# Performance work log

Measured on AMD Instinct MI355X. Metric: run time of the kernel, lower is better.

The kernel has to match this reference:

```python
import jax, jax.numpy as jnp
import numpy as np

D_MODEL = 1024
NUM_HEADS = 16
D_HEAD = D_MODEL // NUM_HEADS


def setup_inputs() -> dict:
    key = jax.random.key(0)
    ks = jax.random.split(key, 9)
    s = 1.0 / np.sqrt(D_MODEL)
    x = jax.random.normal(ks[0], (2, 2048, D_MODEL), dtype=jnp.float32)
    # Linear layers: weight [out, in] (torch convention), bias [out]
    w_q = jax.random.uniform(ks[1], (D_MODEL, D_MODEL), jnp.float32, -s, s)
    b_q = jax.random.uniform(ks[2], (D_MODEL,), jnp.float32, -s, s)
    w_k = jax.random.uniform(ks[3], (D_MODEL, D_MODEL), jnp.float32, -s, s)
    b_k = jax.random.uniform(ks[4], (D_MODEL,), jnp.float32, -s, s)
    w_v = jax.random.uniform(ks[5], (D_MODEL, D_MODEL), jnp.float32, -s, s)
    b_v = jax.random.uniform(ks[6], (D_MODEL,), jnp.float32, -s, s)
    w_o = jax.random.uniform(ks[7], (D_MODEL, D_MODEL), jnp.float32, -s, s)
    b_o = jax.random.uniform(ks[8], (D_MODEL,), jnp.float32, -s, s)
    return {"x": x, "w_q": w_q, "b_q": b_q, "w_k": w_k, "b_k": b_k,
            "w_v": w_v, "b_v": b_v, "w_o": w_o, "b_o": b_o}


def _split_heads(t, b, s):
    # [b, s, d_model] -> [b, h, s, d_head]
    return t.reshape(b, s, NUM_HEADS, D_HEAD).transpose(0, 2, 1, 3)


def reference(x, w_q, b_q, w_k, b_k, w_v, b_v, w_o, b_o):
    b, s, _ = x.shape
    q = _split_heads(x @ w_q.T + b_q, b, s)
    k = _split_heads(x @ w_k.T + b_k, b, s)
    v = _split_heads(x @ w_v.T + b_v, b, s)
    scores = jnp.einsum('bhid,bhjd->bhij', q, k) / jnp.sqrt(jnp.float32(D_HEAD)).astype(x.dtype)
    attn = jax.nn.softmax(scores, axis=-1)
    out = jnp.einsum('bhij,bhjd->bhid', attn, v)
    out = out.transpose(0, 2, 1, 3).reshape(b, s, D_MODEL)
    return out @ w_o.T + b_o
```

## Files before the change

### kernel.cpp

```cpp
#include <hip/hip_runtime.h>
#include <cstddef>
#include <cstdint>
#include <cmath>

#define NH   16
#define DH   64
#define SLEN 2048
#define DM   1024

typedef __bf16          bf16x8   __attribute__((ext_vector_type(8)));
typedef float           f32x4    __attribute__((ext_vector_type(4)));
typedef unsigned short  ushort8  __attribute__((ext_vector_type(8)));
typedef unsigned short  ushort4v __attribute__((ext_vector_type(4)));

__device__ __forceinline__ unsigned short f2bf(float x) {
    union { float f; unsigned u; } v; v.f = x;
    unsigned r = v.u + 0x7fffu + ((v.u >> 16) & 1u);
    return (unsigned short)(r >> 16);
}
__device__ __forceinline__ float bf2f(unsigned short h) {
    union { unsigned u; float f; } v; v.u = ((unsigned)h) << 16;
    return v.f;
}

__device__ __forceinline__ f32x4 mfma16(ushort8 a, ushort8 b, f32x4 c) {
    return __builtin_amdgcn_mfma_f32_16x16x32_bf16(
        __builtin_bit_cast(bf16x8, a), __builtin_bit_cast(bf16x8, b), c, 0, 0, 0);
}

__global__ __launch_bounds__(256)
void convert_hilo(const float* __restrict__ x,
                  const float* __restrict__ wq, const float* __restrict__ wk,
                  const float* __restrict__ wv, const float* __restrict__ wo,
                  unsigned short* __restrict__ xh, unsigned short* __restrict__ xl,
                  unsigned short* __restrict__ wh, unsigned short* __restrict__ wl)
{
    const unsigned c = blockIdx.x * 256 + threadIdx.x;
    const float* src;
    unsigned short *dh, *dl;
    size_t off;
    if (c < 1048576u) {
        src = x; dh = xh; dl = xl; off = c;
    } else {
        unsigned t = c - 1048576u;
        unsigned wsel = t >> 18;
        off = t & 262143u;
        src  = (wsel == 0) ? wq : (wsel == 1) ? wk : (wsel == 2) ? wv : wo;
        dh = wh + ((size_t)wsel << 20);
        dl = wl + ((size_t)wsel << 20);
    }
    float4 v = *(const float4*)(src + off * 4);
    float a[4] = {v.x, v.y, v.z, v.w};
    ushort4v h, l;
    #pragma unroll
    for (int i = 0; i < 4; ++i) {
        unsigned short hi = f2bf(a[i]);
        h[i] = hi;
        l[i] = f2bf(a[i] - bf2f(hi));
    }
    *(ushort4v*)(dh + off * 4) = h;
    *(ushort4v*)(dl + off * 4) = l;
}

template<int MODE>
__global__ __launch_bounds__(256, 1)
void gemm_split(const unsigned short* __restrict__ Ahi, const unsigned short* __restrict__ Alo,
                const unsigned short* __restrict__ Whi, const unsigned short* __restrict__ Wlo,
                const float* __restrict__ bias, float* __restrict__ outF,
                unsigned short* __restrict__ outH, unsigned short* __restrict__ outL)
{
    constexpr int K = DM;
    __shared__ unsigned short sAh[128][40], sAl[128][40], sBh[128][40], sBl[128][40];

    const int tid  = threadIdx.x;
    const int bm   = blockIdx.x * 128;
    const int bn   = blockIdx.y * 128;
    const int wid  = tid >> 6;
    const int lane = tid & 63;
    const int wm   = (wid >> 1) * 64;
    const int wn   = (wid & 1) * 64;

    const int r0 = tid >> 2;
    const int c0 = (tid & 3) * 8;

    const unsigned short* pAh0 = Ahi + (size_t)(bm + r0) * K + c0;
    const unsigned short* pAl0 = Alo + (size_t)(bm + r0) * K + c0;
    const unsigned short* pBh0 = Whi + (size_t)(bn + r0) * K + c0;
    const unsigned short* pBl0 = Wlo + (size_t)(bn + r0) * K + c0;
    const size_t rstep = (size_t)64 * K;

    ushort8 vah0 = *(const ushort8*)(pAh0), vah1 = *(const ushort8*)(pAh0 + rstep);
    ushort8 val0 = *(const ushort8*)(pAl0), val1 = *(const ushort8*)(pAl0 + rstep);
    ushort8 vbh0 = *(const ushort8*)(pBh0), vbh1 = *(const ushort8*)(pBh0 + rstep);
    ushort8 vbl0 = *(const ushort8*)(pBl0), vbl1 = *(const ushort8*)(pBl0 + rstep);

    f32x4 acc[4][4];
    #pragma unroll
    for (int i = 0; i < 4; ++i)
        #pragma unroll
        for (int j = 0; j < 4; ++j)
            acc[i][j] = (f32x4)0.0f;

    const int fr = lane & 15;
    const int kq = (lane >> 4) * 8;

    for (int k0 = 0; k0 < K; k0 += 32) {
        __syncthreads();
        *(ushort8*)&sAh[r0][c0]      = vah0;  *(ushort8*)&sAh[r0 + 64][c0] = vah1;
        *(ushort8*)&sAl[r0][c0]      = val0;  *(ushort8*)&sAl[r0 + 64][c0] = val1;
        *(ushort8*)&sBh[r0][c0]      = vbh0;  *(ushort8*)&sBh[r0 + 64][c0] = vbh1;
        *(ushort8*)&sBl[r0][c0]      = vbl0;  *(ushort8*)&sBl[r0 + 64][c0] = vbl1;
        __syncthreads();

        if (k0 + 32 < K) {
            const int kn = k0 + 32;
            vah0 = *(const ushort8*)(pAh0 + kn);  vah1 = *(const ushort8*)(pAh0 + rstep + kn);
            val0 = *(const ushort8*)(pAl0 + kn);  val1 = *(const ushort8*)(pAl0 + rstep + kn);
            vbh0 = *(const ushort8*)(pBh0 + kn);  vbh1 = *(const ushort8*)(pBh0 + rstep + kn);
            vbl0 = *(const ushort8*)(pBl0 + kn);  vbl1 = *(const ushort8*)(pBl0 + rstep + kn);
        }

        ushort8 afh[4], afl[4], bfh[4], bfl[4];
        #pragma unroll
        for (int i = 0; i < 4; ++i) {
            afh[i] = *(const ushort8*)&sAh[wm + i * 16 + fr][kq];
            afl[i] = *(const ushort8*)&sAl[wm + i * 16 + fr][kq];
            bfh[i] = *(const ushort8*)&sBh[wn + i * 16 + fr][kq];
            bfl[i] = *(const ushort8*)&sBl[wn + i * 16 + fr][kq];
        }

        #pragma unroll
        for (int i = 0; i < 4; ++i)
            #pragma unroll
            for (int j = 0; j < 4; ++j) {
                acc[i][j] = mfma16(afh[i], bfh[j], acc[i][j]);
                acc[i][j] = mfma16(afh[i], bfl[j], acc[i][j]);
                acc[i][j] = mfma16(afl[i], bfh[j], acc[i][j]);
            }
    }

    #pragma unroll
    for (int j = 0; j < 4; ++j) {
        const int n = bn + wn + j * 16 + fr;
        const float bs = bias[n];
        #pragma unroll
        for (int i = 0; i < 4; ++i) {
            #pragma unroll
            for (int q = 0; q < 4; ++q) {
                const int m = bm + wm + i * 16 + (lane >> 4) * 4 + q;
                const float v = acc[i][j][q] + bs;
                if (MODE == 0) {
                    outF[(size_t)m * DM + n] = v;
                } else {
                    const int bb = m >> 11, s = m & 2047, hh = n >> 6, dd = n & 63;
                    size_t idx;
                    if (MODE == 1) idx = ((((size_t)bb * NH + hh) * SLEN) + s) * DH + dd;
                    else           idx = ((((size_t)bb * NH + hh) * DH) + dd) * SLEN + s;
                    const unsigned short vh = f2bf(v);
                    outH[idx] = vh;
                    outL[idx] = f2bf(v - bf2f(vh));
                }
            }
        }
    }
}

__global__ __launch_bounds__(256)
void flash_attn_mfma(const unsigned short* __restrict__ Qh, const unsigned short* __restrict__ Ql,
                     const unsigned short* __restrict__ Kh, const unsigned short* __restrict__ Kl,
                     const unsigned short* __restrict__ Vth, const unsigned short* __restrict__ Vtl,
                     unsigned short* __restrict__ Ohi, unsigned short* __restrict__ Olo)
{
    __shared__ unsigned short sKh[64][72], sKl[64][72], sVh[64][72], sVl[64][72];
    __shared__ float sP[4][16][68];

    const int tid  = threadIdx.x;
    const int wid  = tid >> 6;
    const int lane = tid & 63;
    const int fr   = lane & 15;
    const int g    = lane >> 4;
    const int kq   = g * 8;
    const int q0   = blockIdx.x * 64;
    const int h    = blockIdx.y;
    const int b    = blockIdx.z;
    const size_t hb = (((size_t)b) * NH + h) * (size_t)SLEN * DH;

    const int r0 = tid >> 2;
    const int cq = (tid & 3) * 16;

    ushort8 qh[2], ql[2];
    {
        const size_t qbase = hb + (size_t)(q0 + wid * 16 + fr) * DH;
        qh[0] = *(const ushort8*)&Qh[qbase + kq];
        qh[1] = *(const ushort8*)&Qh[qbase + 32 + kq];
        ql[0] = *(const ushort8*)&Ql[qbase + kq];
        ql[1] = *(const ushort8*)&Ql[qbase + 32 + kq];
    }

    float mx[4], li[4];
    f32x4 acc[4];
    #pragma unroll
    for (int r = 0; r < 4; ++r) { mx[r] = -INFINITY; li[r] = 0.0f; }
    #pragma unroll
    for (int j = 0; j < 4; ++j) acc[j] = (f32x4)0.0f;

    for (int t = 0; t < SLEN / 64; ++t) {
        __syncthreads();
        {
            const size_t kbase = hb + (size_t)(t * 64 + r0) * DH + cq;
            *(ushort8*)&sKh[r0][cq]     = *(const ushort8*)&Kh[kbase];
            *(ushort8*)&sKh[r0][cq + 8] = *(const ushort8*)&Kh[kbase + 8];
            *(ushort8*)&sKl[r0][cq]     = *(const ushort8*)&Kl[kbase];
            *(ushort8*)&sKl[r0][cq + 8] = *(const ushort8*)&Kl[kbase + 8];
            const size_t vbase = hb + (size_t)r0 * SLEN + t * 64 + cq;
            *(ushort8*)&sVh[r0][cq]     = *(const ushort8*)&Vth[vbase];
            *(ushort8*)&sVh[r0][cq + 8] = *(const ushort8*)&Vth[vbase + 8];
            *(ushort8*)&sVl[r0][cq]     = *(const ushort8*)&Vtl[vbase];
            *(ushort8*)&sVl[r0][cq + 8] = *(const ushort8*)&Vtl[vbase + 8];
        }
        __syncthreads();

        f32x4 s[4];
        #pragma unroll
        for (int j = 0; j < 4; ++j) s[j] = (f32x4)0.0f;
        #pragma unroll
        for (int j = 0; j < 4; ++j) {
            #pragma unroll
            for (int ks = 0; ks < 2; ++ks) {
                ushort8 kfh = *(const ushort8*)&sKh[j * 16 + fr][ks * 32 + kq];
                ushort8 kfl = *(const ushort8*)&sKl[j * 16 + fr][ks * 32 + kq];
                s[j] = mfma16(qh[ks], kfh, s[j]);
                s[j] = mfma16(qh[ks], kfl, s[j]);
                s[j] = mfma16(ql[ks], kfh, s[j]);
            }
        }

        float p[4][4];
        #pragma unroll
        for (int r = 0; r < 4; ++r) {
            float sc[4];
            float rm = -INFINITY;
            #pragma unroll
            for (int j = 0; j < 4; ++j) { sc[j] = s[j][r] * 0.125f; rm = fmaxf(rm, sc[j]); }
            #pragma unroll
            for (int off = 1; off < 16; off <<= 1)
                rm = fmaxf(rm, __shfl_xor(rm, off));
            const float mn   = fmaxf(mx[r], rm);
            const float corr = __expf(mx[r] - mn);
            mx[r] = mn;
            float rs = 0.0f;
            #pragma unroll
            for (int j = 0; j < 4; ++j) { p[r][j] = __expf(sc[j] - mn); rs += p[r][j]; }
            #pragma unroll
            for (int off = 1; off < 16; off <<= 1)
                rs += __shfl_xor(rs, off);
            li[r] = li[r] * corr + rs;
            #pragma unroll
            for (int j = 0; j < 4; ++j) acc[j][r] *= corr;
        }

        #pragma unroll
        for (int r = 0; r < 4; ++r)
            #pragma unroll
            for (int j = 0; j < 4; ++j)
                sP[wid][g * 4 + r][j * 16 + fr] = p[r][j];

        #pragma unroll
        for (int ks = 0; ks < 2; ++ks) {
            float4 pa = *(const float4*)&sP[wid][fr][ks * 32 + kq];
            float4 pb = *(const float4*)&sP[wid][fr][ks * 32 + kq + 4];
            float pe[8] = {pa.x, pa.y, pa.z, pa.w, pb.x, pb.y, pb.z, pb.w};
            ushort8 ph, pl;
            #pragma unroll
            for (int e = 0; e < 8; ++e) {
                const unsigned short hh = f2bf(pe[e]);
                ph[e] = hh;
                pl[e] = f2bf(pe[e] - bf2f(hh));
            }
            #pragma unroll
            for (int j = 0; j < 4; ++j) {
                ushort8 vfh = *(const ushort8*)&sVh[j * 16 + fr][ks * 32 + kq];
                ushort8 vfl = *(const ushort8*)&sVl[j * 16 + fr][ks * 32 + kq];
                acc[j] = mfma16(ph, vfh, acc[j]);
                acc[j] = mfma16(ph, vfl, acc[j]);
                acc[j] = mfma16(pl, vfh, acc[j]);
            }
        }
    }

    #pragma unroll
    for (int r = 0; r < 4; ++r) {
        const float inv = 1.0f / li[r];
        const int q = q0 + wid * 16 + g * 4 + r;
        const size_t base = ((size_t)b * SLEN + q) * DM + h * DH;
        #pragma unroll
        for (int j = 0; j < 4; ++j) {
            const float v = acc[j][r] * inv;
            const unsigned short hh = f2bf(v);
            Ohi[base + j * 16 + fr] = hh;
            Olo[base + j * 16 + fr] = f2bf(v - bf2f(hh));
        }
    }
}

extern "C" void kernel_launch(void* const* d_in, const int* in_sizes, int n_in,
                              void* d_out, int out_size, void* d_ws, size_t ws_size,
                              hipStream_t stream)
{
    const float* x   = (const float*)d_in[0];
    const float* w_q = (const float*)d_in[1];
    const float* b_q = (const float*)d_in[2];
    const float* w_k = (const float*)d_in[3];
    const float* b_k = (const float*)d_in[4];
    const float* w_v = (const float*)d_in[5];
    const float* b_v = (const float*)d_in[6];
    const float* w_o = (const float*)d_in[7];
    const float* b_o = (const float*)d_in[8];
    float* out = (float*)d_out;

    char* w = (char*)d_ws;
    const size_t MB = 1024 * 1024;
    unsigned short* xh  = (unsigned short*)(w);
    unsigned short* xl  = (unsigned short*)(w + 8  * MB);
    unsigned short* wh  = (unsigned short*)(w + 16 * MB);
    unsigned short* wl  = (unsigned short*)(w + 24 * MB);
    unsigned short* Qh  = (unsigned short*)(w + 32 * MB);
    unsigned short* Ql  = (unsigned short*)(w + 40 * MB);
    unsigned short* Kh  = (unsigned short*)(w + 48 * MB);
    unsigned short* Kl  = (unsigned short*)(w + 56 * MB);
    unsigned short* Vth = (unsigned short*)(w + 64 * MB);
    unsigned short* Vtl = (unsigned short*)(w + 72 * MB);

    convert_hilo<<<8192, 256, 0, stream>>>(x, w_q, w_k, w_v, w_o, xh, xl, wh, wl);

    dim3 gg(2 * SLEN / 128, DM / 128);
    gemm_split<1><<<gg, 256, 0, stream>>>(xh, xl, wh + 0 * 1048576, wl + 0 * 1048576, b_q, nullptr, Qh, Ql);
    gemm_split<1><<<gg, 256, 0, stream>>>(xh, xl, wh + 1 * 1048576, wl + 1 * 1048576, b_k, nullptr, Kh, Kl);
    gemm_split<2><<<gg, 256, 0, stream>>>(xh, xl, wh + 2 * 1048576, wl + 2 * 1048576, b_v, nullptr, Vth, Vtl);

    dim3 ga(SLEN / 64, NH, 2);
    flash_attn_mfma<<<ga, 256, 0, stream>>>(Qh, Ql, Kh, Kl, Vth, Vtl, xh, xl);

    gemm_split<0><<<gg, 256, 0, stream>>>(xh, xl, wh + 3 * 1048576, wl + 3 * 1048576, b_o, out, nullptr, nullptr);
}
```

Baseline: 489.7 us.

## Shrink attention KV tile, fold softmax scale into Q, coalesce V-transpose stores

The flash-attention kernel now streams 32-key tiles instead of 64, which shrinks shared memory and requests five blocks per CU through launch bounds to raise occupancy. In exchange it runs twice as many barrier-separated loop iterations. The 1/sqrt(d) scale is folded into the Q projection epilogue, so the per-score multiply is gone. The V projection GEMM now transposes its tile through shared memory so the transposed hi/lo bf16 stores become contiguous 16-byte writes instead of scattered 2-byte writes.

```diff
diff --git a/kernel.cpp b/kernel.cpp
--- a/kernel.cpp
+++ b/kernel.cpp
@@ -66,11 +66,15 @@
 __global__ __launch_bounds__(256, 1)
 void gemm_split(const unsigned short* __restrict__ Ahi, const unsigned short* __restrict__ Alo,
                 const unsigned short* __restrict__ Whi, const unsigned short* __restrict__ Wlo,
-                const float* __restrict__ bias, float* __restrict__ outF,
+                const float* __restrict__ bias, const float scale, float* __restrict__ outF,
                 unsigned short* __restrict__ outH, unsigned short* __restrict__ outL)
 {
     constexpr int K = DM;
-    __shared__ unsigned short sAh[128][40], sAl[128][40], sBh[128][40], sBl[128][40];
+    __shared__ __align__(16) char smem[40960];
+    auto sAh = (unsigned short(*)[40])(smem);
+    auto sAl = (unsigned short(*)[40])(smem + 10240);
+    auto sBh = (unsigned short(*)[40])(smem + 20480);
+    auto sBl = (unsigned short(*)[40])(smem + 30720);
 
     const int tid  = threadIdx.x;
     const int bm   = blockIdx.x * 128;
@@ -139,6 +143,55 @@
             }
     }
 
+    if (MODE == 2) {
+        float (*sT)[132] = (float(*)[132])smem;
+        const int bb2 = bm >> 11;
+        const int sm  = bm & 2047;
+        #pragma unroll
+        for (int ph = 0; ph < 2; ++ph) {
+            __syncthreads();
+            if ((wid & 1) == ph) {
+                #pragma unroll
+                for (int j = 0; j < 4; ++j) {
+                    const float bs = bias[bn + ph * 64 + j * 16 + fr];
+                    #pragma unroll
+                    for (int i = 0; i < 4; ++i) {
+                        float4 v4;
+                        v4.x = acc[i][j][0] + bs;
+                        v4.y = acc[i][j][1] + bs;
+                        v4.z = acc[i][j][2] + bs;
+                        v4.w = acc[i][j][3] + bs;
+                        *(float4*)&sT[j * 16 + fr][wm + i * 16 + (lane >> 4) * 4] = v4;
+                    }
+                }
+            }
+            __syncthreads();
+            #pragma unroll
+            for (int half = 0; half < 2; ++half) {
+                const int r  = (tid >> 3) + half * 32;
+                const int cc = (tid & 7) * 16;
+                const int n  = bn + ph * 64 + r;
+                const size_t gb = ((((size_t)bb2 * NH + (n >> 6)) * DH) + (n & 63)) * SLEN + sm + cc;
+                #pragma unroll
+                for (int u = 0; u < 2; ++u) {
+                    float4 f0 = *(const float4*)&sT[r][cc + u * 8];
+                    float4 f1 = *(const float4*)&sT[r][cc + u * 8 + 4];
+                    float fe[8] = {f0.x, f0.y, f0.z, f0.w, f1.x, f1.y, f1.z, f1.w};
+                    ushort8 hv, lv;
+                    #pragma unroll
+                    for (int e = 0; e < 8; ++e) {
+                        const unsigned short vh = f2bf(fe[e]);
+                        hv[e] = vh;
+                        lv[e] = f2bf(fe[e] - bf2f(vh));
+                    }
+                    *(ushort8*)(outH + gb + u * 8) = hv;
+                    *(ushort8*)(outL + gb + u * 8) = lv;
+                }
+            }
+        }
+        return;
+    }
+
     #pragma unroll
     for (int j = 0; j < 4; ++j) {
         const int n = bn + wn + j * 16 + fr;
@@ -148,14 +201,12 @@
             #pragma unroll
             for (int q = 0; q < 4; ++q) {
                 const int m = bm + wm + i * 16 + (lane >> 4) * 4 + q;
-                const float v = acc[i][j][q] + bs;
+                const float v = (acc[i][j][q] + bs) * scale;
                 if (MODE == 0) {
                     outF[(size_t)m * DM + n] = v;
                 } else {
                     const int bb = m >> 11, s = m & 2047, hh = n >> 6, dd = n & 63;
-                    size_t idx;
-                    if (MODE == 1) idx = ((((size_t)bb * NH + hh) * SLEN) + s) * DH + dd;
-                    else           idx = ((((size_t)bb * NH + hh) * DH) + dd) * SLEN + s;
+                    const size_t idx = ((((size_t)bb * NH + hh) * SLEN) + s) * DH + dd;
                     const unsigned short vh = f2bf(v);
                     outH[idx] = vh;
                     outL[idx] = f2bf(v - bf2f(vh));
@@ -165,14 +216,15 @@
     }
 }
 
-__global__ __launch_bounds__(256)
+__global__ __launch_bounds__(256, 5)
 void flash_attn_mfma(const unsigned short* __restrict__ Qh, const unsigned short* __restrict__ Ql,
                      const unsigned short* __restrict__ Kh, const unsigned short* __restrict__ Kl,
                      const unsigned short* __restrict__ Vth, const unsigned short* __restrict__ Vtl,
                      unsigned short* __restrict__ Ohi, unsigned short* __restrict__ Olo)
 {
-    __shared__ unsigned short sKh[64][72], sKl[64][72], sVh[64][72], sVl[64][72];
-    __shared__ float sP[4][16][68];
+    __shared__ unsigned short sKh[32][72], sKl[32][72];
+    __shared__ unsigned short sVh[64][40], sVl[64][40];
+    __shared__ float sP[4][16][36];
 
     const int tid  = threadIdx.x;
     const int wid  = tid >> 6;
@@ -185,8 +237,8 @@
     const int b    = blockIdx.z;
     const size_t hb = (((size_t)b) * NH + h) * (size_t)SLEN * DH;
 
-    const int r0 = tid >> 2;
-    const int cq = (tid & 3) * 16;
+    const int kr = tid & 31, kc = (tid >> 5) * 8;
+    const int vr = tid >> 2, vc = (tid & 3) * 8;
 
     ushort8 qh[2], ql[2];
     {
@@ -204,27 +256,22 @@
     #pragma unroll
     for (int j = 0; j < 4; ++j) acc[j] = (f32x4)0.0f;
 
-    for (int t = 0; t < SLEN / 64; ++t) {
+    for (int t = 0; t < SLEN / 32; ++t) {
         __syncthreads();
         {
-            const size_t kbase = hb + (size_t)(t * 64 + r0) * DH + cq;
-            *(ushort8*)&sKh[r0][cq]     = *(const ushort8*)&Kh[kbase];
-            *(ushort8*)&sKh[r0][cq + 8] = *(const ushort8*)&Kh[kbase + 8];
-            *(ushort8*)&sKl[r0][cq]     = *(const ushort8*)&Kl[kbase];
-            *(ushort8*)&sKl[r0][cq + 8] = *(const ushort8*)&Kl[kbase + 8];
-            const size_t vbase = hb + (size_t)r0 * SLEN + t * 64 + cq;
-            *(ushort8*)&sVh[r0][cq]     = *(const ushort8*)&Vth[vbase];
-            *(ushort8*)&sVh[r0][cq + 8] = *(const ushort8*)&Vth[vbase + 8];
-            *(ushort8*)&sVl[r0][cq]     = *(const ushort8*)&Vtl[vbase];
-            *(ushort8*)&sVl[r0][cq + 8] = *(const ushort8*)&Vtl[vbase + 8];
+            const size_t kb = hb + (size_t)(t * 32 + kr) * DH + kc;
+            *(ushort8*)&sKh[kr][kc] = *(const ushort8*)&Kh[kb];
+            *(ushort8*)&sKl[kr][kc] = *(const ushort8*)&Kl[kb];
+            const size_t vb = hb + (size_t)vr * SLEN + t * 32 + vc;
+            *(ushort8*)&sVh[vr][vc] = *(const ushort8*)&Vth[vb];
+            *(ushort8*)&sVl[vr][vc] = *(const ushort8*)&Vtl[vb];
         }
         __syncthreads();
 
-        f32x4 s[4];
-        #pragma unroll
-        for (int j = 0; j < 4; ++j) s[j] = (f32x4)0.0f;
-        #pragma unroll
-        for (int j = 0; j < 4; ++j) {
+        f32x4 s[2];
+        s[0] = (f32x4)0.0f; s[1] = (f32x4)0.0f;
+        #pragma unroll
+        for (int j = 0; j < 2; ++j) {
             #pragma unroll
             for (int ks = 0; ks < 2; ++ks) {
                 ushort8 kfh = *(const ushort8*)&sKh[j * 16 + fr][ks * 32 + kq];
@@ -235,55 +282,52 @@
             }
         }
 
-        float p[4][4];
+        float p[4][2];
         #pragma unroll
         for (int r = 0; r < 4; ++r) {
-            float sc[4];
-            float rm = -INFINITY;
-            #pragma unroll
-            for (int j = 0; j < 4; ++j) { sc[j] = s[j][r] * 0.125f; rm = fmaxf(rm, sc[j]); }
+            const float v0 = s[0][r], v1 = s[1][r];
+            float rm = fmaxf(v0, v1);
             #pragma unroll
             for (int off = 1; off < 16; off <<= 1)
                 rm = fmaxf(rm, __shfl_xor(rm, off));
             const float mn   = fmaxf(mx[r], rm);
             const float corr = __expf(mx[r] - mn);
             mx[r] = mn;
-            float rs = 0.0f;
-            #pragma unroll
-            for (int j = 0; j < 4; ++j) { p[r][j] = __expf(sc[j] - mn); rs += p[r][j]; }
+            p[r][0] = __expf(v0 - mn);
+            p[r][1] = __expf(v1 - mn);
+            float rs = p[r][0] + p[r][1];
             #pragma unroll
             for (int off = 1; off < 16; off <<= 1)
                 rs += __shfl_xor(rs, off);
             li[r] = li[r] * corr + rs;
             #pragma unroll
-            for (int j = 0; j < 4; ++j) acc[j][r] *= corr;
+            for (int jd = 0; jd < 4; ++jd) acc[jd][r] *= corr;
         }
 
         #pragma unroll
         for (int r = 0; r < 4; ++r)
             #pragma unroll
-            for (int j = 0; j < 4; ++j)
+            for (int j = 0; j < 2; ++j)
                 sP[wid][g * 4 + r][j * 16 + fr] = p[r][j];
 
-        #pragma unroll
-        for (int ks = 0; ks < 2; ++ks) {
-            float4 pa = *(const float4*)&sP[wid][fr][ks * 32 + kq];
-            float4 pb = *(const float4*)&sP[wid][fr][ks * 32 + kq + 4];
+        {
+            float4 pa = *(const float4*)&sP[wid][fr][kq];
+            float4 pb = *(const float4*)&sP[wid][fr][kq + 4];
             float pe[8] = {pa.x, pa.y, pa.z, pa.w, pb.x, pb.y, pb.z, pb.w};
             ushort8 ph, pl;
             #pragma unroll
             for (int e = 0; e < 8; ++e) {
-                const unsigned short hh = f2bf(pe[e]);
-                ph[e] = hh;
-                pl[e] = f2bf(pe[e] - bf2f(hh));
-            }
-            #pragma unroll
-            for (int j = 0; j < 4; ++j) {
-                ushort8 vfh = *(const ushort8*)&sVh[j * 16 + fr][ks * 32 + kq];
-                ushort8 vfl = *(const ushort8*)&sVl[j * 16 + fr][ks * 32 + kq];
-                acc[j] = mfma16(ph, vfh, acc[j]);
-                acc[j] = mfma16(ph, vfl, acc[j]);
-                acc[j] = mfma16(pl, vfh, acc[j]);
+                const unsigned short hh2 = f2bf(pe[e]);
+                ph[e] = hh2;
+                pl[e] = f2bf(pe[e] - bf2f(hh2));
+            }
+            #pragma unroll
+            for (int jd = 0; jd < 4; ++jd) {
+                ushort8 vfh = *(const ushort8*)&sVh[jd * 16 + fr][kq];
+                ushort8 vfl = *(const ushort8*)&sVl[jd * 16 + fr][kq];
+                acc[jd] = mfma16(ph, vfh, acc[jd]);
+                acc[jd] = mfma16(ph, vfl, acc[jd]);
+                acc[jd] = mfma16(pl, vfh, acc[jd]);
             }
         }
     }
@@ -294,11 +338,11 @@
         const int q = q0 + wid * 16 + g * 4 + r;
         const size_t base = ((size_t)b * SLEN + q) * DM + h * DH;
         #pragma unroll
-        for (int j = 0; j < 4; ++j) {
-            const float v = acc[j][r] * inv;
-            const unsigned short hh = f2bf(v);
-            Ohi[base + j * 16 + fr] = hh;
-            Olo[base + j * 16 + fr] = f2bf(v - bf2f(hh));
+        for (int jd = 0; jd < 4; ++jd) {
+            const float v = acc[jd][r] * inv;
+            const unsigned short hh2 = f2bf(v);
+            Ohi[base + jd * 16 + fr] = hh2;
+            Olo[base + jd * 16 + fr] = f2bf(v - bf2f(hh2));
         }
     }
 }
@@ -334,12 +378,12 @@
     convert_hilo<<<8192, 256, 0, stream>>>(x, w_q, w_k, w_v, w_o, xh, xl, wh, wl);
 
     dim3 gg(2 * SLEN / 128, DM / 128);
-    gemm_split<1><<<gg, 256, 0, stream>>>(xh, xl, wh + 0 * 1048576, wl + 0 * 1048576, b_q, nullptr, Qh, Ql);
-    gemm_split<1><<<gg, 256, 0, stream>>>(xh, xl, wh + 1 * 1048576, wl + 1 * 1048576, b_k, nullptr, Kh, Kl);
-    gemm_split<2><<<gg, 256, 0, stream>>>(xh, xl, wh + 2 * 1048576, wl + 2 * 1048576, b_v, nullptr, Vth, Vtl);
+    gemm_split<1><<<gg, 256, 0, stream>>>(xh, xl, wh + 0 * 1048576, wl + 0 * 1048576, b_q, 0.125f, nullptr, Qh, Ql);
+    gemm_split<1><<<gg, 256, 0, stream>>>(xh, xl, wh + 1 * 1048576, wl + 1 * 1048576, b_k, 1.0f,   nullptr, Kh, Kl);
+    gemm_split<2><<<gg, 256, 0, stream>>>(xh, xl, wh + 2 * 1048576, wl + 2 * 1048576, b_v, 1.0f,   nullptr, Vth, Vtl);
 
     dim3 ga(SLEN / 64, NH, 2);
     flash_attn_mfma<<<ga, 256, 0, stream>>>(Qh, Ql, Kh, Kl, Vth, Vtl, xh, xl);
 
-    gemm_split<0><<<gg, 256, 0, stream>>>(xh, xl, wh + 3 * 1048576, wl + 3 * 1048576, b_o, out, nullptr, nullptr);
-}
+    gemm_split<0><<<gg, 256, 0, stream>>>(xh, xl, wh + 3 * 1048576, wl + 3 * 1048576, b_o, 1.0f, out, nullptr, nullptr);
+}
```

Result: faster. 464.9 us (-5.1%).
